# Kernel optimization log

Hardware: AMD Instinct MI355X
Metric: run time of the kernel (lower is better)

The kernel has to match this reference:

```python
import jax, jax.numpy as jnp
import numpy as np

N_DST = 100_000
N_SRC = 200_000
DEG = 16            # fixed avg degree -> E = N_DST*DEG
E = N_DST * DEG
P, K, W = 16, 256, 8  # num_parts, codebook entries, part width; feat_dim = P*W = 128
F_IN = P * W
F_OUT = 128


def setup_inputs() -> dict:
    key = jax.random.key(0)
    k1, k2, k3, k4, k5, k6, k7 = jax.random.split(key, 7)
    codes = jax.random.randint(k1, (N_SRC, P), 0, K, dtype=jnp.int32)
    indices = jax.random.randint(k2, (E,), 0, N_SRC, dtype=jnp.int32)
    indptr = (jnp.arange(N_DST + 1, dtype=jnp.int32) * DEG)
    h_self = jax.random.normal(k3, (N_DST, F_IN), dtype=jnp.float32)
    codebook = jax.random.normal(k4, (P, K, W), dtype=jnp.float32)
    W_neigh = jax.random.normal(k5, (F_OUT, F_IN), dtype=jnp.float32) * (1.0 / np.sqrt(F_IN))
    W_self = jax.random.normal(k6, (F_OUT, F_IN), dtype=jnp.float32) * (1.0 / np.sqrt(F_IN))
    b_self = jax.random.normal(k7, (F_OUT,), dtype=jnp.float32) * 0.01
    return {"codes": codes, "indices": indices, "indptr": indptr, "h_self": h_self,
            "codebook": codebook, "W_neigh": W_neigh, "W_self": W_self, "b_self": b_self}


def reference(codes, indices, indptr, h_self, codebook, W_neigh, W_self, b_self):
    n_dst = indptr.shape[0] - 1
    n_edges = indices.shape[0]
    # --- VQ decompress: codebook[p, codes[n, p]] -> [N_src, P, W] -> [N_src, F_IN]
    feat = codebook[jnp.arange(P)[None, :], codes]          # [N_src, P, W]
    feat = feat.reshape(feat.shape[0], F_IN)                # [N_src, F_IN]
    # --- CSR(CSC) mean SpMM over neighbors
    # dst id of each edge from indptr (jit-safe, static E)
    dst_ids = jnp.searchsorted(indptr, jnp.arange(n_edges, dtype=indptr.dtype), side="right") - 1
    gathered = feat[indices]                                 # [E, F_IN] (irregular gather)
    summed = jax.ops.segment_sum(gathered, dst_ids, num_segments=n_dst)  # [N_dst, F_IN]
    deg = jnp.diff(indptr).astype(summed.dtype)
    h_neigh = summed / jnp.maximum(deg, 1.0)[:, None]        # mean aggregation
    # --- linear combine: fc_neigh(h_neigh) + fc_self(h_self)
    rst = h_neigh @ W_neigh.T + h_self @ W_self.T + b_self[None, :]
    return rst
```

## Files before the change

kernel.cpp:

```cpp
#include <hip/hip_runtime.h>
#include <stdint.h>

constexpr int N_DST = 100000;
constexpr int N_SRC = 200000;
constexpr int DEG   = 16;
constexpr int PP    = 16;
constexpr int KK    = 256;
constexpr int WW    = 8;
constexpr int F_IN  = 128;
constexpr int F_OUT = 128;
constexpr int NSTRIPE = N_DST / 16;

typedef __attribute__((ext_vector_type(8))) short short8;
typedef __attribute__((ext_vector_type(4))) float floatx4;

__device__ __forceinline__ unsigned short f2bf(float f) {
    unsigned int u = __float_as_uint(f);
    unsigned int r = (u + 0x7FFFu + ((u >> 16) & 1u)) >> 16;
    return (unsigned short)r;
}
__device__ __forceinline__ float bf_lo(unsigned int q) {
    return __uint_as_float(q << 16);
}
__device__ __forceinline__ float bf_hi(unsigned int q) {
    return __uint_as_float(q & 0xFFFF0000u);
}


__global__ __launch_bounds__(512, 2) void fused_kernel(
    const int* __restrict__ codes, const int* __restrict__ indices,
    const float* __restrict__ codebook, const float* __restrict__ h_self,
    const float* __restrict__ Wn, const float* __restrict__ Ws,
    const float* __restrict__ b_self, float* __restrict__ out)
{
    __shared__ __align__(16) unsigned short scb[KK * PP * WW];
    __shared__ __align__(16) unsigned short wlds[F_OUT][256];
    __shared__ __align__(16) unsigned short tbuf[8][16][128];

    const int tid  = threadIdx.x;
    const int wv   = tid >> 6;
    const int lane = tid & 63;
    const int quad = lane >> 4;
    const int r    = lane & 15;
    const int p    = lane & 15;
    const int sub  = lane >> 4;

    {
        const float4* cb4 = (const float4*)codebook;
        ushort4* s4 = (ushort4*)scb;
        #pragma unroll
        for (int it = 0; it < 16; ++it) {
            const int i = tid + it * 512;
            const float4 v = cb4[i];
            const int pp_  = i >> 9;
            const int k    = (i >> 1) & 255;
            const int half = i & 1;
            ushort4 w;
            w.x = f2bf(v.x); w.y = f2bf(v.y); w.z = f2bf(v.z); w.w = f2bf(v.w);
            s4[((k << 4) | pp_) * 2 + half] = w;
        }
    }

    #pragma unroll
    for (int j = 0; j < 16; ++j) {
        const int fi = tid + j * 512;
        const int o  = fi >> 6;
        const int fc = fi & 63;
        const int k  = fc * 4;
        const float* src = (k < 128) ? (Wn + o * 128 + k)
                                     : (Ws + o * 128 + (k - 128));
        const float4 v = *(const float4*)src;
        ushort4 w;
        w.x = f2bf(v.x); w.y = f2bf(v.y); w.z = f2bf(v.z); w.w = f2bf(v.w);
        const int ch = fc >> 1;
        const int hc = fc & 1;
        *(ushort4*)&wlds[o][((ch ^ (o & 7)) << 3) + hc * 4] = w;
    }

    float bsv[8];
    #pragma unroll
    for (int cg = 0; cg < 8; ++cg) bsv[cg] = b_self[cg * 16 + r];

    __syncthreads();

    auto issue_codes = [&](int sidx, int* cc) {
        #pragma unroll
        for (int e = 0; e < 16; ++e) {
            const int s = __shfl(sidx, (lane & 48) | e, 64);
            cc[e] = codes[s * PP + p];
        }
    };
    auto do_unit = [&](const int* cc, int u) {
        float ga[8];
        #pragma unroll
        for (int i = 0; i < 8; ++i) ga[i] = 0.f;
        #pragma unroll
        for (int e = 0; e < 16; ++e) {
            const uint4 q = *(const uint4*)(scb + (((cc[e] << 4) | p) << 3));
            ga[0] += bf_lo(q.x); ga[1] += bf_hi(q.x);
            ga[2] += bf_lo(q.y); ga[3] += bf_hi(q.y);
            ga[4] += bf_lo(q.z); ga[5] += bf_hi(q.z);
            ga[6] += bf_lo(q.w); ga[7] += bf_hi(q.w);
        }
        const int ridx = u * 4 + sub;
        uint4 o4;
        o4.x = (unsigned int)f2bf(ga[0] * 0.0625f) | ((unsigned int)f2bf(ga[1] * 0.0625f) << 16);
        o4.y = (unsigned int)f2bf(ga[2] * 0.0625f) | ((unsigned int)f2bf(ga[3] * 0.0625f) << 16);
        o4.z = (unsigned int)f2bf(ga[4] * 0.0625f) | ((unsigned int)f2bf(ga[5] * 0.0625f) << 16);
        o4.w = (unsigned int)f2bf(ga[6] * 0.0625f) | ((unsigned int)f2bf(ga[7] * 0.0625f) << 16);
        *(uint4*)&tbuf[wv][ridx][(p ^ (ridx & 7)) << 3] = o4;
    };

    for (int s = blockIdx.x * 8 + wv; s < NSTRIPE; s += gridDim.x * 8) {
        const int S0 = s * 16;

        const int sidx0 = indices[(S0     ) * DEG + lane];
        const int sidx1 = indices[(S0 +  4) * DEG + lane];
        const int sidx2 = indices[(S0 +  8) * DEG + lane];
        const int sidx3 = indices[(S0 + 12) * DEG + lane];
        float4 hsv[8];
        #pragma unroll
        for (int k2 = 0; k2 < 4; ++k2) {
            const float* hp = h_self + (size_t)(S0 + r) * F_IN + k2 * 32 + quad * 8;
            hsv[k2 * 2]     = *(const float4*)hp;
            hsv[k2 * 2 + 1] = *(const float4*)(hp + 4);
        }
        __builtin_amdgcn_sched_barrier(0);

        int c0[16], c1[16], c2[16], c3[16];
        issue_codes(sidx0, c0);
        issue_codes(sidx1, c1);
        __builtin_amdgcn_sched_barrier(0);
        do_unit(c0, 0);
        issue_codes(sidx2, c2);
        __builtin_amdgcn_sched_barrier(0);
        do_unit(c1, 1);
        issue_codes(sidx3, c3);
        __builtin_amdgcn_sched_barrier(0);
        do_unit(c2, 2);
        do_unit(c3, 3);

        short8 af4[4];
        #pragma unroll
        for (int k2 = 0; k2 < 4; ++k2) {
            union { short8 v; unsigned short u[8]; } f;
            f.u[0] = f2bf(hsv[k2 * 2].x);     f.u[1] = f2bf(hsv[k2 * 2].y);
            f.u[2] = f2bf(hsv[k2 * 2].z);     f.u[3] = f2bf(hsv[k2 * 2].w);
            f.u[4] = f2bf(hsv[k2 * 2 + 1].x); f.u[5] = f2bf(hsv[k2 * 2 + 1].y);
            f.u[6] = f2bf(hsv[k2 * 2 + 1].z); f.u[7] = f2bf(hsv[k2 * 2 + 1].w);
            af4[k2] = f.v;
        }

        floatx4 acc[8];
        #pragma unroll
        for (int cg = 0; cg < 8; ++cg) acc[cg] = (floatx4)(0.f);
        #pragma unroll
        for (int kt = 0; kt < 8; ++kt) {
            short8 a;
            if (kt < 4) {
                a = *(const short8*)&tbuf[wv][r][((4 * kt + quad) ^ (r & 7)) << 3];
            } else {
                a = af4[kt - 4];
            }
            #pragma unroll
            for (int cg = 0; cg < 8; ++cg) {
                const int o = cg * 16 + r;
                const short8 b = *(const short8*)
                    &wlds[o][(((kt * 4 + quad) ^ (o & 7)) << 3)];
                acc[cg] = __builtin_amdgcn_mfma_f32_16x16x32_bf16(a, b, acc[cg], 0, 0, 0);
            }
        }

        #pragma unroll
        for (int cg = 0; cg < 8; ++cg) {
            #pragma unroll
            for (int e = 0; e < 4; ++e) {
                const int d = S0 + quad * 4 + e;
                out[(size_t)d * F_OUT + cg * 16 + r] = acc[cg][e] + bsv[cg];
            }
        }
    }
}

extern "C" void kernel_launch(void* const* d_in, const int* in_sizes, int n_in,
                              void* d_out, int out_size, void* d_ws, size_t ws_size,
                              hipStream_t stream) {
    const int*   codes    = (const int*)d_in[0];
    const int*   indices  = (const int*)d_in[1];
    const float* h_self   = (const float*)d_in[3];
    const float* codebook = (const float*)d_in[4];
    const float* W_neigh  = (const float*)d_in[5];
    const float* W_self   = (const float*)d_in[6];
    const float* b_self   = (const float*)d_in[7];
    float*       out      = (float*)d_out;

    fused_kernel<<<256, 512, 0, stream>>>(codes, indices, codebook, h_self,
                                          W_neigh, W_self, b_self, out);
}
```

Baseline: 155.6 us.

## Pre-pack codes to bytes in a side kernel to shrink gather traffic

Adds a pre-pass kernel that compresses the int32 code table into one byte per part in the workspace. The fused kernel then gathers 16-byte packed code rows instead of 64-byte int rows. Edge indices are now loaded as int4 vectors per sub-group instead of being broadcast with shuffles. The aim is to cut the irregular gather bandwidth, at the cost of an extra launch and a full read of the codes array each call. The old path is kept as a fallback when no workspace is available.

```diff
diff --git a/kernel.cpp b/kernel.cpp
--- a/kernel.cpp
+++ b/kernel.cpp
@@ -27,8 +27,21 @@
 }
 
 
+__global__ __launch_bounds__(256) void pack_codes(
+    const int* __restrict__ codes, unsigned int* __restrict__ pc32)
+{
+    constexpr int N32 = N_SRC * PP / 4;
+    for (int i = blockIdx.x * 256 + threadIdx.x; i < N32; i += gridDim.x * 256) {
+        const int4 v = ((const int4*)codes)[i];
+        pc32[i] = (unsigned int)(v.x & 255) | ((unsigned int)(v.y & 255) << 8)
+                | ((unsigned int)(v.z & 255) << 16) | ((unsigned int)(v.w & 255) << 24);
+    }
+}
+
+template <bool PACKED>
 __global__ __launch_bounds__(512, 2) void fused_kernel(
-    const int* __restrict__ codes, const int* __restrict__ indices,
+    const int* __restrict__ codes, const unsigned char* __restrict__ pcodes,
+    const int* __restrict__ indices,
     const float* __restrict__ codebook, const float* __restrict__ h_self,
     const float* __restrict__ Wn, const float* __restrict__ Ws,
     const float* __restrict__ b_self, float* __restrict__ out)
@@ -83,13 +96,6 @@
 
     __syncthreads();
 
-    auto issue_codes = [&](int sidx, int* cc) {
-        #pragma unroll
-        for (int e = 0; e < 16; ++e) {
-            const int s = __shfl(sidx, (lane & 48) | e, 64);
-            cc[e] = codes[s * PP + p];
-        }
-    };
     auto do_unit = [&](const int* cc, int u) {
         float ga[8];
         #pragma unroll
@@ -111,13 +117,31 @@
         *(uint4*)&tbuf[wv][ridx][(p ^ (ridx & 7)) << 3] = o4;
     };
 
+    auto load_srcs = [&](int S0, int u, int* sa) {
+        const int* base = indices + (size_t)(S0 + u * 4 + sub) * DEG;
+        #pragma unroll
+        for (int j = 0; j < 4; ++j) {
+            const int4 t = ((const int4*)base)[j];
+            sa[j * 4 + 0] = t.x; sa[j * 4 + 1] = t.y;
+            sa[j * 4 + 2] = t.z; sa[j * 4 + 3] = t.w;
+        }
+    };
+    auto issue_pcodes = [&](const int* sa, int* cc) {
+        #pragma unroll
+        for (int e = 0; e < 16; ++e)
+            cc[e] = pcodes[(size_t)sa[e] * PP + p];
+    };
+    auto issue_codes_shfl = [&](int sidx, int* cc) {
+        #pragma unroll
+        for (int e = 0; e < 16; ++e) {
+            const int s = __shfl(sidx, (lane & 48) | e, 64);
+            cc[e] = codes[s * PP + p];
+        }
+    };
+
     for (int s = blockIdx.x * 8 + wv; s < NSTRIPE; s += gridDim.x * 8) {
         const int S0 = s * 16;
 
-        const int sidx0 = indices[(S0     ) * DEG + lane];
-        const int sidx1 = indices[(S0 +  4) * DEG + lane];
-        const int sidx2 = indices[(S0 +  8) * DEG + lane];
-        const int sidx3 = indices[(S0 + 12) * DEG + lane];
         float4 hsv[8];
         #pragma unroll
         for (int k2 = 0; k2 < 4; ++k2) {
@@ -125,20 +149,45 @@
             hsv[k2 * 2]     = *(const float4*)hp;
             hsv[k2 * 2 + 1] = *(const float4*)(hp + 4);
         }
-        __builtin_amdgcn_sched_barrier(0);
 
         int c0[16], c1[16], c2[16], c3[16];
-        issue_codes(sidx0, c0);
-        issue_codes(sidx1, c1);
-        __builtin_amdgcn_sched_barrier(0);
-        do_unit(c0, 0);
-        issue_codes(sidx2, c2);
-        __builtin_amdgcn_sched_barrier(0);
-        do_unit(c1, 1);
-        issue_codes(sidx3, c3);
-        __builtin_amdgcn_sched_barrier(0);
-        do_unit(c2, 2);
-        do_unit(c3, 3);
+        if constexpr (PACKED) {
+            int sa0[16], sa1[16];
+            load_srcs(S0, 0, sa0);
+            load_srcs(S0, 1, sa1);
+            __builtin_amdgcn_sched_barrier(0);
+            issue_pcodes(sa0, c0);
+            issue_pcodes(sa1, c1);
+            __builtin_amdgcn_sched_barrier(0);
+            int sa2[16], sa3[16];
+            load_srcs(S0, 2, sa2);
+            load_srcs(S0, 3, sa3);
+            do_unit(c0, 0);
+            issue_pcodes(sa2, c2);
+            __builtin_amdgcn_sched_barrier(0);
+            do_unit(c1, 1);
+            issue_pcodes(sa3, c3);
+            __builtin_amdgcn_sched_barrier(0);
+            do_unit(c2, 2);
+            do_unit(c3, 3);
+        } else {
+            const int sidx0 = indices[(S0     ) * DEG + lane];
+            const int sidx1 = indices[(S0 +  4) * DEG + lane];
+            const int sidx2 = indices[(S0 +  8) * DEG + lane];
+            const int sidx3 = indices[(S0 + 12) * DEG + lane];
+            __builtin_amdgcn_sched_barrier(0);
+            issue_codes_shfl(sidx0, c0);
+            issue_codes_shfl(sidx1, c1);
+            __builtin_amdgcn_sched_barrier(0);
+            do_unit(c0, 0);
+            issue_codes_shfl(sidx2, c2);
+            __builtin_amdgcn_sched_barrier(0);
+            do_unit(c1, 1);
+            issue_codes_shfl(sidx3, c3);
+            __builtin_amdgcn_sched_barrier(0);
+            do_unit(c2, 2);
+            do_unit(c3, 3);
+        }
 
         short8 af4[4];
         #pragma unroll
@@ -194,6 +243,14 @@
     const float* b_self   = (const float*)d_in[7];
     float*       out      = (float*)d_out;
 
-    fused_kernel<<<256, 512, 0, stream>>>(codes, indices, codebook, h_self,
-                                          W_neigh, W_self, b_self, out);
-}
+    const size_t need = (size_t)N_SRC * PP;
+    if (d_ws != nullptr && ws_size >= need) {
+        unsigned char* pc = (unsigned char*)d_ws;
+        pack_codes<<<1024, 256, 0, stream>>>(codes, (unsigned int*)pc);
+        fused_kernel<true><<<256, 512, 0, stream>>>(codes, pc, indices, codebook,
+                                                    h_self, W_neigh, W_self, b_self, out);
+    } else {
+        fused_kernel<false><<<256, 512, 0, stream>>>(codes, nullptr, indices, codebook,
+                                                     h_self, W_neigh, W_self, b_self, out);
+    }
+}
```

After: 156.0 us. Within noise of the previous version (+0.2%).
